# Kernel tuning notes

Hardware: AMD Instinct MI355X
Metric: run time of the kernel (lower is better)

Reference implementation:

```python
import jax, jax.numpy as jnp
import numpy as np

MARGIN = 1.0
N_NODES = 8192
EMBED_DIM = 128
N_COMM = 100


def setup_inputs() -> dict:
    key = jax.random.key(0)
    k1, k2 = jax.random.split(key)
    embeddings = jax.random.normal(k1, (N_NODES, EMBED_DIM), dtype=jnp.float32)
    communities = jax.random.randint(k2, (N_NODES,), 0, N_COMM, dtype=jnp.int64)
    return {"embeddings": embeddings, "communities": communities}


def _cdist(x):
    # Euclidean pairwise distances, sqrt made grad-safe at 0.
    sq = jnp.sum(x * x, axis=1)
    d2 = sq[:, None] + sq[None, :] - 2.0 * (x @ x.T)
    d2 = jnp.maximum(d2, 0.0)
    return jnp.where(d2 > 0, jnp.sqrt(jnp.where(d2 > 0, d2, 1.0)), 0.0)


def reference(embeddings, communities):
    n = embeddings.shape[0]
    dist = _cdist(embeddings)                              # (n, n)
    same = communities[:, None] == communities[None, :]    # (n, n)
    pos_mask = same & ~jnp.eye(n, dtype=bool)              # positives: same comm, j != i
    neg_mask = ~same                                       # negatives: any other community
    inf = jnp.array(jnp.inf, dist.dtype)
    # hardest (closest) negative per anchor row
    min_neg = jnp.min(jnp.where(neg_mask, dist, inf), axis=1)   # (n,)
    has_neg = jnp.any(neg_mask, axis=1)                         # (n,)
    # triplet margin over every (anchor, positive) pair
    tl = jnp.maximum(dist - min_neg[:, None] + MARGIN, 0.0)     # (n, n)
    valid = pos_mask & has_neg[:, None]
    total = jnp.sum(jnp.where(valid, tl, 0.0))
    count = jnp.sum(valid)
    # reduction='mean' over valid triplets; 0.0 if no valid triplets / single community
    return jnp.where(count > 0, total / count.astype(total.dtype), jnp.zeros((), total.dtype))
```

## Files before the change

### kernel.cpp

```cpp
#include <hip/hip_runtime.h>

#define N_NODES 8192
#define DIM     128
#define N_COMM  100
#define MARGIN  1.0f
#define NPOSBLK (N_COMM * 4)

#define RP_STR   68

typedef __attribute__((ext_vector_type(8)))  short bf16x8;
typedef __attribute__((ext_vector_type(16))) float f32x16;

__device__ inline unsigned short f32_to_bf16_rne(float f) {
    unsigned u = __float_as_uint(f);
    unsigned r = u + 0x7fffu + ((u >> 16) & 1u);
    return (unsigned short)(r >> 16);
}

__global__ __launch_bounds__(256)
void prep_kernel(const float* __restrict__ x,
                 const int* __restrict__ comm,
                 unsigned short* __restrict__ xh,
                 float* __restrict__ sq,
                 unsigned int* __restrict__ min_d2,
                 int* __restrict__ offs,
                 int* __restrict__ members,
                 double* __restrict__ psum,
                 unsigned int* __restrict__ pcnt,
                 unsigned int* __restrict__ done) {
    __shared__ int scnt[N_COMM];
    __shared__ int scur[N_COMM];
    const int tid = threadIdx.x;

    if (blockIdx.x < 2048) {
        int row  = blockIdx.x * 4 + (tid >> 6);
        int lane = tid & 63;
        const float* p = x + (size_t)row * DIM;
        float v0 = p[lane], v1 = p[lane + 64];
        unsigned short h0 = f32_to_bf16_rne(v0), h1 = f32_to_bf16_rne(v1);
        size_t base = (size_t)row * DIM;
        xh[base + lane] = h0;  xh[base + 64 + lane] = h1;
        float s = v0 * v0 + v1 * v1;
        #pragma unroll
        for (int off = 32; off > 0; off >>= 1) s += __shfl_down(s, off);
        if (lane == 0) {
            sq[row] = s;
            min_d2[row] = 0x7f800000u;
        }
        return;
    }

    if (tid < N_COMM) {
        scnt[tid] = 0;
        psum[tid] = 0.0;
        pcnt[tid] = 0u;
    }
    if (tid == 0) *done = 0u;
    __syncthreads();
    for (int i = tid; i < N_NODES; i += 256) atomicAdd(&scnt[comm[i]], 1);
    __syncthreads();
    if (tid == 0) {
        int acc = 0;
        for (int c = 0; c < N_COMM; ++c) { scur[c] = acc; offs[c] = acc; acc += scnt[c]; }
        offs[N_COMM] = acc;
    }
    __syncthreads();
    for (int i = tid; i < N_NODES; i += 256) {
        int p = atomicAdd(&scur[comm[i]], 1);
        members[p] = i;
    }
}

__global__ __launch_bounds__(256, 4)
void minneg_mfma_kernel(const unsigned short* __restrict__ xh,
                        const int* __restrict__ comm,
                        const float* __restrict__ sq,
                        unsigned int* __restrict__ min_d2) {
    __shared__ __align__(16) float rowpart[128][RP_STR];
    __shared__ float colpart[128][2];

    const int b = blockIdx.x;
    int bx = (int)((sqrtf(8.f * (float)b + 1.f) - 1.f) * 0.5f);
    while ((bx + 1) * (bx + 2) / 2 <= b) ++bx;
    while (bx * (bx + 1) / 2 > b) --bx;
    const int by = b - bx * (bx + 1) / 2;

    const int tid  = threadIdx.x;
    const int lane = tid & 63;
    const int w    = tid >> 6;
    const int wr   = w >> 1, wc = w & 1;
    const int lr   = lane & 31;
    const int lh   = lane >> 5;
    const int i0   = bx * 128;
    const int j0   = by * 128;

    f32x16 acc[2][2];
    #pragma unroll
    for (int g = 0; g < 2; ++g)
        #pragma unroll
        for (int h = 0; h < 2; ++h)
            #pragma unroll
            for (int e = 0; e < 16; ++e) acc[g][h][e] = 0.f;

    const unsigned short* pa = xh + (size_t)(i0 + wr * 64 + lr) * DIM + lh * 8;
    const unsigned short* pb = xh + (size_t)(j0 + wc * 64 + lr) * DIM + lh * 8;

    #pragma unroll
    for (int ks = 0; ks < 8; ++ks) {
        const int ko = ks * 16;
        bf16x8 a[2], bb[2];
        a[0]  = *(const bf16x8*)&pa[ko];
        a[1]  = *(const bf16x8*)&pa[32 * DIM + ko];
        bb[0] = *(const bf16x8*)&pb[ko];
        bb[1] = *(const bf16x8*)&pb[32 * DIM + ko];
        #pragma unroll
        for (int g = 0; g < 2; ++g)
            #pragma unroll
            for (int h = 0; h < 2; ++h)
                acc[g][h] = __builtin_amdgcn_mfma_f32_32x32x16_bf16(
                    a[g], bb[h], acc[g][h], 0, 0, 0);
    }

    const float FINF = __uint_as_float(0x7f800000u);
    float cminh[2] = {FINF, FINF};

    #pragma unroll
    for (int g = 0; g < 2; ++g) {
        float rmin[16];
        #pragma unroll
        for (int e = 0; e < 16; ++e) rmin[e] = FINF;

        #pragma unroll
        for (int h = 0; h < 2; ++h) {
            int colt = wc * 64 + h * 32 + lr;
            int j  = j0 + colt;
            int cj = comm[j];
            float sqj = sq[j];
            float cm = FINF;
            #pragma unroll
            for (int q = 0; q < 4; ++q) {
                int rb = i0 + wr * 64 + g * 32 + 4 * lh + 8 * q;
                int4   civ = *(const int4*)&comm[rb];
                float4 sqv = *(const float4*)&sq[rb];
                const int cvals[4] = {civ.x, civ.y, civ.z, civ.w};
                const float svals[4] = {sqv.x, sqv.y, sqv.z, sqv.w};
                #pragma unroll
                for (int t = 0; t < 4; ++t) {
                    float d2 = fmaxf(svals[t] + sqj - 2.f * acc[g][h][q * 4 + t], 0.f);
                    if (cvals[t] != cj) {
                        cm = fminf(cm, d2);
                        rmin[q * 4 + t] = fminf(rmin[q * 4 + t], d2);
                    }
                }
            }
            cminh[h] = fminf(cminh[h], cm);
        }

        #pragma unroll
        for (int q = 0; q < 4; ++q)
            #pragma unroll
            for (int t = 0; t < 4; ++t) {
                int rowl = wr * 64 + g * 32 + 4 * lh + 8 * q + t;
                rowpart[rowl][wc * 32 + lr] = rmin[q * 4 + t];
            }
    }

    #pragma unroll
    for (int h = 0; h < 2; ++h)
        cminh[h] = fminf(cminh[h], __shfl_xor(cminh[h], 32));
    if (lh == 0) {
        #pragma unroll
        for (int h = 0; h < 2; ++h)
            colpart[wc * 64 + h * 32 + lr][wr] = cminh[h];
    }
    __syncthreads();
    if (tid < 128) {
        float m = FINF;
        #pragma unroll
        for (int k = 0; k < 16; ++k) {
            float4 vv = *(const float4*)&rowpart[tid][k * 4];
            m = fminf(m, fminf(fminf(vv.x, vv.y), fminf(vv.z, vv.w)));
        }
        float cm = fminf(colpart[tid][0], colpart[tid][1]);
        atomicMin(&min_d2[i0 + tid], __float_as_uint(m));
        atomicMin(&min_d2[j0 + tid], __float_as_uint(cm));
    }
}

__global__ __launch_bounds__(256)
void pos_wave_kernel(const unsigned short* __restrict__ xh,
                     const float* __restrict__ sq,
                     const unsigned int* __restrict__ min_d2,
                     const int* __restrict__ offs,
                     const int* __restrict__ members,
                     double* __restrict__ psum,
                     unsigned int* __restrict__ pcnt,
                     unsigned int* __restrict__ done,
                     float* __restrict__ out) {
    __shared__ double       sred[4];
    __shared__ unsigned int cred[4];
    __shared__ unsigned int lastflag;

    const int c    = blockIdx.x >> 2;
    const int tid  = threadIdx.x;
    const int lane = tid & 63;
    const int w    = tid >> 6;
    const int lr   = lane & 31;
    const int lh   = lane >> 5;
    const int wsub = ((blockIdx.x & 3) << 2) | w;

    const int beg  = offs[c], end = offs[c + 1];
    const int size = end - beg;

    if (size > 0) {
        const int m = (size + 31) >> 5;

        float tsum = 0.f;
        unsigned int tcnt = 0u;

        for (int idx = wsub; idx < m * m; idx += 16) {
            int ti = idx / m, tj = idx - ti * m;
            int s0 = ti * 32, t0 = tj * 32;
            int slotA = s0 + lr, slotB = t0 + lr;
            int nodeA = members[beg + (slotA < size ? slotA : size - 1)];
            int nodeB = members[beg + (slotB < size ? slotB : size - 1)];

            float sqa_own = sq[nodeA];
            unsigned mb = min_d2[nodeA];
            float mn_own = (mb == 0x7f800000u) ? -1.f
                         : sqrtf(fmaxf(__uint_as_float(mb), 0.f));
            float sqb = sq[nodeB];

            const unsigned short* pA = xh + (size_t)nodeA * DIM;
            const unsigned short* pB = xh + (size_t)nodeB * DIM;

            f32x16 a0;
            #pragma unroll
            for (int e = 0; e < 16; ++e) a0[e] = 0.f;

            #pragma unroll
            for (int ks = 0; ks < 8; ++ks) {
                const int ko = ks * 16 + lh * 8;
                bf16x8 av = *(const bf16x8*)&pA[ko];
                bf16x8 bv = *(const bf16x8*)&pB[ko];
                a0 = __builtin_amdgcn_mfma_f32_32x32x16_bf16(av, bv, a0, 0, 0, 0);
            }

            #pragma unroll
            for (int q = 0; q < 4; ++q)
                #pragma unroll
                for (int t = 0; t < 4; ++t) {
                    int r = 4 * lh + 8 * q + t;
                    float sqa = __shfl(sqa_own, r);
                    float mn  = __shfl(mn_own, r);
                    int e = q * 4 + t;
                    if ((s0 + r < size) && (slotB < size) &&
                        (s0 + r != slotB) && (mn >= 0.f)) {
                        float d2   = sqa + sqb - 2.f * a0[e];
                        float dist = sqrtf(fmaxf(d2, 0.f));
                        tsum += fmaxf(dist - mn + MARGIN, 0.f);
                        tcnt += 1u;
                    }
                }
        }

        #pragma unroll
        for (int off = 32; off > 0; off >>= 1) {
            tsum += __shfl_down(tsum, off);
            tcnt += __shfl_down(tcnt, off);
        }
        if (lane == 0 && tcnt > 0u) {
            atomicAdd(&psum[c], (double)tsum);
            atomicAdd(&pcnt[c], tcnt);
        }
    }

    __syncthreads();
    if (tid == 0) {
        __threadfence();
        unsigned r = atomicAdd(done, 1u);
        lastflag = (r == NPOSBLK - 1u) ? 1u : 0u;
    }
    __syncthreads();
    if (lastflag) {
        double s = 0.0; unsigned int cc = 0u;
        for (int b2 = tid; b2 < N_COMM; b2 += 256) {
            s  += atomicAdd(&psum[b2], 0.0);
            cc += atomicAdd(&pcnt[b2], 0u);
        }
        #pragma unroll
        for (int off = 32; off > 0; off >>= 1) {
            s  += __shfl_down(s, off);
            cc += __shfl_down(cc, off);
        }
        if (lane == 0) { sred[w] = s; cred[w] = cc; }
        __syncthreads();
        if (tid == 0) {
            double st = sred[0] + sred[1] + sred[2] + sred[3];
            unsigned int ct = cred[0] + cred[1] + cred[2] + cred[3];
            out[0] = (ct > 0u) ? (float)(st / (double)ct) : 0.f;
        }
    }
}

extern "C" void kernel_launch(void* const* d_in, const int* in_sizes, int n_in,
                              void* d_out, int out_size, void* d_ws, size_t ws_size,
                              hipStream_t stream) {
    const float* x    = (const float*)d_in[0];
    const int*   comm = (const int*)d_in[1];
    float*       out  = (float*)d_out;

    char* ws = (char*)d_ws;
    float*          sq      = (float*)(ws);
    unsigned int*   min_d2  = (unsigned int*)(ws + 32768);
    int*            offs    = (int*)(ws + 65536);
    int*            members = (int*)(ws + 66048);
    double*         psum    = (double*)(ws + 98816);
    unsigned int*   pcnt    = (unsigned int*)(ws + 99840);
    unsigned int*   done    = (unsigned int*)(ws + 100352);
    unsigned short* xh      = (unsigned short*)(ws + 100864);

    prep_kernel<<<2049, 256, 0, stream>>>(x, comm, xh, sq, min_d2,
                                          offs, members, psum, pcnt, done);

    const int ntri = (N_NODES / 128) * (N_NODES / 128 + 1) / 2;
    minneg_mfma_kernel<<<ntri, 256, 0, stream>>>(xh, comm, sq, min_d2);

    pos_wave_kernel<<<NPOSBLK, 256, 0, stream>>>(xh, sq, min_d2, offs,
                                                 members, psum, pcnt, done, out);
}
```

Measured before the change: 129.1 us.

## Store bf16 embeddings in MFMA-fragment-major layout for coalesced loads

The prep kernel now writes the bf16 copy of the embeddings in a tiled layout. Each 32-row group and 16-wide k-slice forms a contiguous 512-element chunk ordered exactly as the 32x32x16 MFMA operand fragment. Both the min-negative kernel and the positive-pair kernel read this layout, so each wave's operand load becomes one contiguous 1 KB access instead of 32 strided row segments. In exchange the prep kernel's stores become scattered, and the pos kernel's gathered rows still touch 8 separate chunks.

```diff
diff --git a/kernel.cpp b/kernel.cpp
--- a/kernel.cpp
+++ b/kernel.cpp
@@ -20,7 +20,7 @@
 __global__ __launch_bounds__(256)
 void prep_kernel(const float* __restrict__ x,
                  const int* __restrict__ comm,
-                 unsigned short* __restrict__ xh,
+                 unsigned short* __restrict__ xhf,
                  float* __restrict__ sq,
                  unsigned int* __restrict__ min_d2,
                  int* __restrict__ offs,
@@ -38,8 +38,11 @@
         const float* p = x + (size_t)row * DIM;
         float v0 = p[lane], v1 = p[lane + 64];
         unsigned short h0 = f32_to_bf16_rne(v0), h1 = f32_to_bf16_rne(v1);
-        size_t base = (size_t)row * DIM;
-        xh[base + lane] = h0;  xh[base + 64 + lane] = h1;
+        size_t e1 = ((size_t)(row >> 5) * 8 + (lane >> 4)) * 512
+                  + ((size_t)((row & 31) + 32 * ((lane >> 3) & 1))) * 8
+                  + (lane & 7);
+        xhf[e1]        = h0;
+        xhf[e1 + 2048] = h1;
         float s = v0 * v0 + v1 * v1;
         #pragma unroll
         for (int off = 32; off > 0; off >>= 1) s += __shfl_down(s, off);
@@ -72,7 +75,7 @@
 }
 
 __global__ __launch_bounds__(256, 4)
-void minneg_mfma_kernel(const unsigned short* __restrict__ xh,
+void minneg_mfma_kernel(const unsigned short* __restrict__ xhf,
                         const int* __restrict__ comm,
                         const float* __restrict__ sq,
                         unsigned int* __restrict__ min_d2) {
@@ -102,23 +105,24 @@
             #pragma unroll
             for (int e = 0; e < 16; ++e) acc[g][h][e] = 0.f;
 
-    const unsigned short* pa = xh + (size_t)(i0 + wr * 64 + lr) * DIM + lh * 8;
-    const unsigned short* pb = xh + (size_t)(j0 + wc * 64 + lr) * DIM + lh * 8;
+    const int pA = bx * 4 + wr * 2;
+    const int pB = by * 4 + wc * 2;
+    const unsigned short* a0p = xhf + ((size_t)pA       * 8 * 512) + (size_t)lane * 8;
+    const unsigned short* a1p = xhf + ((size_t)(pA + 1) * 8 * 512) + (size_t)lane * 8;
+    const unsigned short* b0p = xhf + ((size_t)pB       * 8 * 512) + (size_t)lane * 8;
+    const unsigned short* b1p = xhf + ((size_t)(pB + 1) * 8 * 512) + (size_t)lane * 8;
 
     #pragma unroll
     for (int ks = 0; ks < 8; ++ks) {
-        const int ko = ks * 16;
-        bf16x8 a[2], bb[2];
-        a[0]  = *(const bf16x8*)&pa[ko];
-        a[1]  = *(const bf16x8*)&pa[32 * DIM + ko];
-        bb[0] = *(const bf16x8*)&pb[ko];
-        bb[1] = *(const bf16x8*)&pb[32 * DIM + ko];
-        #pragma unroll
-        for (int g = 0; g < 2; ++g)
-            #pragma unroll
-            for (int h = 0; h < 2; ++h)
-                acc[g][h] = __builtin_amdgcn_mfma_f32_32x32x16_bf16(
-                    a[g], bb[h], acc[g][h], 0, 0, 0);
+        const int o = ks * 512;
+        bf16x8 a0 = *(const bf16x8*)&a0p[o];
+        bf16x8 a1 = *(const bf16x8*)&a1p[o];
+        bf16x8 b0 = *(const bf16x8*)&b0p[o];
+        bf16x8 b1 = *(const bf16x8*)&b1p[o];
+        acc[0][0] = __builtin_amdgcn_mfma_f32_32x32x16_bf16(a0, b0, acc[0][0], 0, 0, 0);
+        acc[0][1] = __builtin_amdgcn_mfma_f32_32x32x16_bf16(a0, b1, acc[0][1], 0, 0, 0);
+        acc[1][0] = __builtin_amdgcn_mfma_f32_32x32x16_bf16(a1, b0, acc[1][0], 0, 0, 0);
+        acc[1][1] = __builtin_amdgcn_mfma_f32_32x32x16_bf16(a1, b1, acc[1][1], 0, 0, 0);
     }
 
     const float FINF = __uint_as_float(0x7f800000u);
@@ -188,7 +192,7 @@
 }
 
 __global__ __launch_bounds__(256)
-void pos_wave_kernel(const unsigned short* __restrict__ xh,
+void pos_wave_kernel(const unsigned short* __restrict__ xhf,
                      const float* __restrict__ sq,
                      const unsigned int* __restrict__ min_d2,
                      const int* __restrict__ offs,
@@ -231,8 +235,10 @@
                          : sqrtf(fmaxf(__uint_as_float(mb), 0.f));
             float sqb = sq[nodeB];
 
-            const unsigned short* pA = xh + (size_t)nodeA * DIM;
-            const unsigned short* pB = xh + (size_t)nodeB * DIM;
+            const unsigned short* pA = xhf + (size_t)(nodeA >> 5) * 4096
+                                     + ((size_t)((nodeA & 31) + 32 * lh)) * 8;
+            const unsigned short* pB = xhf + (size_t)(nodeB >> 5) * 4096
+                                     + ((size_t)((nodeB & 31) + 32 * lh)) * 8;
 
             f32x16 a0;
             #pragma unroll
@@ -240,9 +246,8 @@
 
             #pragma unroll
             for (int ks = 0; ks < 8; ++ks) {
-                const int ko = ks * 16 + lh * 8;
-                bf16x8 av = *(const bf16x8*)&pA[ko];
-                bf16x8 bv = *(const bf16x8*)&pB[ko];
+                bf16x8 av = *(const bf16x8*)&pA[ks * 512];
+                bf16x8 bv = *(const bf16x8*)&pB[ks * 512];
                 a0 = __builtin_amdgcn_mfma_f32_32x32x16_bf16(av, bv, a0, 0, 0, 0);
             }
 
@@ -318,14 +323,14 @@
     double*         psum    = (double*)(ws + 98816);
     unsigned int*   pcnt    = (unsigned int*)(ws + 99840);
     unsigned int*   done    = (unsigned int*)(ws + 100352);
-    unsigned short* xh      = (unsigned short*)(ws + 100864);
-
-    prep_kernel<<<2049, 256, 0, stream>>>(x, comm, xh, sq, min_d2,
+    unsigned short* xhf     = (unsigned short*)(ws + 100864);
+
+    prep_kernel<<<2049, 256, 0, stream>>>(x, comm, xhf, sq, min_d2,
                                           offs, members, psum, pcnt, done);
 
     const int ntri = (N_NODES / 128) * (N_NODES / 128 + 1) / 2;
-    minneg_mfma_kernel<<<ntri, 256, 0, stream>>>(xh, comm, sq, min_d2);
-
-    pos_wave_kernel<<<NPOSBLK, 256, 0, stream>>>(xh, sq, min_d2, offs,
+    minneg_mfma_kernel<<<ntri, 256, 0, stream>>>(xhf, comm, sq, min_d2);
+
+    pos_wave_kernel<<<NPOSBLK, 256, 0, stream>>>(xhf, sq, min_d2, offs,
                                                  members, psum, pcnt, done, out);
 }
```

Measured after the change: 110.2 us. -14.6%, faster.
